# Performance work log

Measured on AMD Instinct MI355X. Metric: run time of the kernel, lower is better.

## Reference

```python
import jax, jax.numpy as jnp
import numpy as np

L, N, E, H, D = 2048, 4, 1024, 16, 128  # seq, batch, embed, heads, proj_dim
HD = E // H                             # head_dim = 64
SIGMA = 1.0
EPS = 1e-6


def setup_inputs() -> dict:
    key = jax.random.key(0)
    ks = jax.random.split(key, 13)
    w = lambda i, shape: jax.random.normal(ks[i], shape, jnp.float32) * 0.02
    return {
        "query": jax.random.normal(ks[0], (L, N, E), jnp.float32),
        "key": jax.random.normal(ks[1], (L, N, E), jnp.float32),
        "value": jax.random.normal(ks[2], (L, N, E), jnp.float32),
        "wq": w(3, (E, E)), "bq": jnp.zeros((E,), jnp.float32),
        "wk": w(4, (E, E)), "bk": jnp.zeros((E,), jnp.float32),
        "wv": w(5, (E, E)), "bv": jnp.zeros((E,), jnp.float32),
        "wo": w(6, (E, E)), "bo": jnp.zeros((E,), jnp.float32),
        "random_matrices": SIGMA * jax.random.normal(ks[7], (H, D, HD), jnp.float32),
    }


def random_project(x, rm):
    # x: (L, N, H, HD), rm: (H, D, HD) -> phi: (N*H, L, 2D)
    scale = 1.0 / np.sqrt(2 * D).astype(np.float32)
    xn = x / jnp.maximum(jnp.linalg.norm(x, axis=-1, keepdims=True), 1e-12)
    xt = jnp.einsum('lnhe,hde->lnhd', xn, rm)
    phi = scale * jnp.concatenate([jnp.exp(xt), jnp.exp(-xt)], axis=-1)  # (L,N,H,2D)
    # faithful to torch .contiguous().view(-1, L, 2D): plain row-major reshape
    return phi.reshape(N * H, L, 2 * D)


def causal_product(phi_q, phi_k, v):
    # phi_q, phi_k: (B, L, 2D); v: (B, L, HD)
    B = phi_q.shape[0]
    def step(carry, inp):
        S, z = carry            # S: (B, 2D, HD) running kv; z: (B, 2D) running k-sum
        qk, kk, vv = inp        # (B, 2D), (B, 2D), (B, HD)
        S = S + kk[:, :, None] * vv[:, None, :]
        z = z + kk
        num = jnp.einsum('bd,bdh->bh', qk, S)
        den = jnp.einsum('bd,bd->b', qk, z)
        return (S, z), num / (den[:, None] + EPS)
    init = (jnp.zeros((B, 2 * D, HD), phi_q.dtype), jnp.zeros((B, 2 * D), phi_q.dtype))
    xs = (jnp.swapaxes(phi_q, 0, 1), jnp.swapaxes(phi_k, 0, 1), jnp.swapaxes(v, 0, 1))
    _, out = jax.lax.scan(step, init, xs)   # out: (L, B, HD)
    return jnp.swapaxes(out, 0, 1)          # (B, L, HD)


def reference(query, key, value, wq, bq, wk, bk, wv, bv, wo, bo, random_matrices):
    q = query @ wq.T + bq
    k = key @ wk.T + bk
    v = value @ wv.T + bv
    q = q.reshape(L, N, H, HD)
    k = k.reshape(L, N, H, HD)
    v = jnp.swapaxes(v.reshape(L, N * H, HD), 0, 1)   # (B=N*H, L, HD)
    phi_q = random_project(q, random_matrices)        # (B, L, 2D)
    phi_k = random_project(k, random_matrices)
    attn = causal_product(phi_q, phi_k, v)            # (B, L, HD)
    attn = jnp.swapaxes(attn, 0, 1).reshape(L, N, E)
    return attn @ wo.T + bo
```

## Files before the change

kernel.cpp:

```cpp
#include <hip/hip_runtime.h>
#include <math.h>


typedef unsigned short u16;
typedef unsigned int u32;
using f32x4v  = __attribute__((ext_vector_type(4))) float;
using f32x16v = __attribute__((ext_vector_type(16))) float;
using s16x8   = __attribute__((ext_vector_type(8))) short;

__device__ __forceinline__ float bf2f(u16 u) { return __uint_as_float(((u32)u) << 16); }
__device__ __forceinline__ u16 f2bf(float x) {
    u32 b = __float_as_uint(x);
    b += 0x7fff + ((b >> 16) & 1);
    return (u16)(b >> 16);
}
__device__ __forceinline__ u32 cvtpk(float lo, float hi) {
    u32 r;
    asm("v_cvt_pk_bf16_f32 %0, %1, %2" : "=v"(r) : "v"(lo), "v"(hi));
    return r;
}
__device__ __forceinline__ void gload_lds16(const void* g, void* l) {
    __builtin_amdgcn_global_load_lds(
        (const __attribute__((address_space(1))) void*)g,
        (__attribute__((address_space(3))) void*)l, 16, 0, 0);
}

__global__ __launch_bounds__(256) void cvt_x_bf16(
    const float* __restrict__ q, const float* __restrict__ k,
    const float* __restrict__ v, u16* __restrict__ dst)
{
    const float* src = (blockIdx.y == 0) ? q : (blockIdx.y == 1) ? k : v;
    u16* d = dst + (size_t)blockIdx.y * 8388608;
    const size_t i = ((size_t)blockIdx.x * 256 + threadIdx.x) * 8;
    const float4 a = *(const float4*)(src + i);
    const float4 b = *(const float4*)(src + i + 4);
    u16 o[8] = {f2bf(a.x), f2bf(a.y), f2bf(a.z), f2bf(a.w),
                f2bf(b.x), f2bf(b.y), f2bf(b.z), f2bf(b.w)};
    *(uint4*)(d + i) = *(uint4*)o;
}

__global__ __launch_bounds__(256) void cvt_w_bf16(
    const float* __restrict__ w0, const float* __restrict__ w1,
    const float* __restrict__ w2, const float* __restrict__ w3,
    u16* __restrict__ dst)
{
    const float* src = (blockIdx.y == 0) ? w0 : (blockIdx.y == 1) ? w1
                     : (blockIdx.y == 2) ? w2 : w3;
    u16* d = dst + (size_t)blockIdx.y * 1048576;
    const size_t i = ((size_t)blockIdx.x * 256 + threadIdx.x) * 8;
    const float4 a = *(const float4*)(src + i);
    const float4 b = *(const float4*)(src + i + 4);
    u16 o[8] = {f2bf(a.x), f2bf(a.y), f2bf(a.z), f2bf(a.w),
                f2bf(b.x), f2bf(b.y), f2bf(b.z), f2bf(b.w)};
    *(uint4*)(d + i) = *(uint4*)o;
}

template<int OMODE>
__device__ __forceinline__ void gemm_body(
    const u16* __restrict__ A, const u16* __restrict__ Bw,
    const float* __restrict__ bias, void* __restrict__ Cp,
    int m0, int n0, u16* As, u16* Bs)
{
    const int t = threadIdx.x;
    const int wid = t >> 6, lane = t & 63;
    const int wr = wid >> 1, wc = wid & 1;
    const int l15 = lane & 15, l4 = lane >> 4;

    f32x4v acc[4][4];
#pragma unroll
    for (int i = 0; i < 4; ++i)
#pragma unroll
        for (int j = 0; j < 4; ++j)
#pragma unroll
            for (int e = 0; e < 4; ++e) acc[i][j][e] = 0.f;

    const int srow = wid * 32 + (lane >> 2);
    const int scol = (lane & 3) * 8;
    const u16* ga0 = A  + (size_t)(m0 + srow) * 1024 + scol;
    const u16* ga1 = ga0 + 16 * 1024;
    const u16* gb0 = Bw + (size_t)(n0 + srow) * 1024 + scol;
    const u16* gb1 = gb0 + 16 * 1024;
    u16* la0 = &As[wid * 1024];
    u16* la1 = la0 + 512;
    u16* lb0 = &Bs[wid * 1024];
    u16* lb1 = lb0 + 512;

    for (int k0 = 0; k0 < 1024; k0 += 32) {
        __syncthreads();
        gload_lds16(ga0 + k0, la0);
        gload_lds16(ga1 + k0, la1);
        gload_lds16(gb0 + k0, lb0);
        gload_lds16(gb1 + k0, lb1);
        __syncthreads();
        s16x8 af[4], bfr[4];
#pragma unroll
        for (int fi = 0; fi < 4; ++fi)
            af[fi] = *(const s16x8*)&As[(wr * 64 + fi * 16 + l15) * 32 + l4 * 8];
#pragma unroll
        for (int fj = 0; fj < 4; ++fj)
            bfr[fj] = *(const s16x8*)&Bs[(wc * 64 + fj * 16 + l15) * 32 + l4 * 8];
#pragma unroll
        for (int fi = 0; fi < 4; ++fi)
#pragma unroll
            for (int fj = 0; fj < 4; ++fj)
                acc[fi][fj] = __builtin_amdgcn_mfma_f32_16x16x32_bf16(af[fi], bfr[fj], acc[fi][fj], 0, 0, 0);
    }

    const int rl = l4 * 4, cl = l15;
    float bvals[4];
#pragma unroll
    for (int fj = 0; fj < 4; ++fj) bvals[fj] = bias[n0 + wc * 64 + fj * 16 + cl];
#pragma unroll
    for (int fi = 0; fi < 4; ++fi)
#pragma unroll
        for (int j = 0; j < 4; ++j) {
            const size_t m = m0 + wr * 64 + fi * 16 + rl + j;
#pragma unroll
            for (int fj = 0; fj < 4; ++fj) {
                const int n = n0 + wc * 64 + fj * 16 + cl;
                const float v = acc[fi][fj][j] + bvals[fj];
                if (OMODE == 0)      ((float*)Cp)[m * 1024 + n] = v;
                else if (OMODE == 1) ((u16*)Cp)[m * 1024 + n] = f2bf(v);
                else {
                    ((u16*)Cp)[((size_t)((m & 3) * 16 + (n >> 6)) * 64 + (n & 63)) * 2048 + (m >> 2)] = f2bf(v);
                }
            }
        }
}

template<int OMODE>
__global__ __launch_bounds__(256) void gemm_bf16(
    const u16* __restrict__ A, const u16* __restrict__ Bw,
    const float* __restrict__ bias, void* __restrict__ Cp)
{
    __shared__ __align__(16) u16 As[4096];
    __shared__ __align__(16) u16 Bs[4096];
    gemm_body<OMODE>(A, Bw, bias, Cp, blockIdx.x * 128, blockIdx.y * 128, As, Bs);
}

__global__ __launch_bounds__(256) void gemm_qk(
    const u16* __restrict__ xq, const u16* __restrict__ wq, const float* __restrict__ bq, u16* __restrict__ qp,
    const u16* __restrict__ xk, const u16* __restrict__ wk, const float* __restrict__ bk, u16* __restrict__ kp)
{
    __shared__ __align__(16) u16 As[4096];
    __shared__ __align__(16) u16 Bs[4096];
    const bool isq = (blockIdx.z == 0);
    gemm_body<1>(isq ? xq : xk, isq ? wq : wk, isq ? bq : bk, isq ? (void*)qp : (void*)kp,
                 blockIdx.x * 128, blockIdx.y * 128, As, Bs);
}

__global__ __launch_bounds__(256) void rand_project2(
    const u16* __restrict__ QP, const u16* __restrict__ KP,
    const float* __restrict__ RM, u16* __restrict__ PHIQ, u16* __restrict__ PHIK)
{
    const u16* X  = (blockIdx.z == 0) ? QP : KP;
    u16* PHI      = (blockIdx.z == 0) ? PHIQ : PHIK;
    __shared__ float Xs[64][68];
    __shared__ float RMs[128][68];
    __shared__ float rsc[64];
    const int h  = blockIdx.x;
    const int r0 = blockIdx.y * 64;
    const int t  = threadIdx.x;
#pragma unroll
    for (int i = 0; i < 2; ++i) {
        const int lin = t + i * 256;
        const int r = lin >> 3, c8 = (lin & 7) * 8;
        const uint4 v = *(const uint4*)(X + (size_t)(r0 + r) * 1024 + h * 64 + c8);
        const u16* pv = (const u16*)&v;
#pragma unroll
        for (int e = 0; e < 8; ++e) Xs[r][c8 + e] = bf2f(pv[e]);
    }
#pragma unroll
    for (int i = 0; i < 32; ++i) {
        const int lin = t + i * 256;
        const int d = lin >> 6, c = lin & 63;
        RMs[d][c] = RM[((size_t)h * 128 + d) * 64 + c];
    }
    __syncthreads();
    if (t < 64) {
        float s = 0.f;
#pragma unroll
        for (int c = 0; c < 64; ++c) { const float v = Xs[t][c]; s += v * v; }
        rsc[t] = 1.f / fmaxf(sqrtf(s), 1e-12f);
    }
    __syncthreads();
    const int rr = (t >> 4) * 4;
    const int dc = t & 15;
    float acc[4][8];
#pragma unroll
    for (int i = 0; i < 4; ++i)
#pragma unroll
        for (int j = 0; j < 8; ++j) acc[i][j] = 0.f;
    for (int c = 0; c < 64; c += 4) {
        float4 xv[4], rv[8];
#pragma unroll
        for (int i = 0; i < 4; ++i) xv[i] = *(const float4*)&Xs[rr + i][c];
#pragma unroll
        for (int j = 0; j < 8; ++j) rv[j] = *(const float4*)&RMs[dc + 16 * j][c];
#pragma unroll
        for (int i = 0; i < 4; ++i)
#pragma unroll
            for (int j = 0; j < 8; ++j)
                acc[i][j] += xv[i].x*rv[j].x + xv[i].y*rv[j].y + xv[i].z*rv[j].z + xv[i].w*rv[j].w;
    }
#pragma unroll
    for (int i = 0; i < 4; ++i) {
        const float sc = rsc[rr + i];
        const size_t base = ((size_t)(r0 + rr + i) * 16 + h) * 256;
#pragma unroll
        for (int j = 0; j < 8; ++j) {
            const float xt = acc[i][j] * sc;
            const int d = dc + 16 * j;
            PHI[base + d]       = f2bf(0.0625f * expf(xt));
            PHI[base + 128 + d] = f2bf(0.0625f * expf(-xt));
        }
    }
}

__global__ __launch_bounds__(256) void chunk_state_mfma(
    const u16* __restrict__ PHIK, const u16* __restrict__ VPT, float* __restrict__ ST)
{
    __shared__ __align__(16) u16 Ks[64 * 136];
    __shared__ float zlds[16][132];
    const int b = blockIdx.x;
    const int c = blockIdx.y >> 1;
    const int dh = blockIdx.y & 1;
    const int t = threadIdx.x;
    const int wid = t >> 6, lane = t & 63;
    const int l15 = lane & 15, l4 = lane >> 4;
    const int wr = wid >> 1, wc = wid & 1;

    const size_t R0 = (size_t)b * 2048 + (size_t)c * 256;
    const int rgrp = t >> 4, d08 = (t & 15) * 8;

    float zpart[8];
#pragma unroll
    for (int i = 0; i < 8; ++i) zpart[i] = 0.f;

    f32x4v acc[2][4];
#pragma unroll
    for (int i = 0; i < 2; ++i)
#pragma unroll
        for (int j = 0; j < 4; ++j)
#pragma unroll
            for (int e = 0; e < 4; ++e) acc[i][j][e] = 0.f;

    for (int stage = 0; stage < 4; ++stage) {
        __syncthreads();
#pragma unroll
        for (int j = 0; j < 4; ++j) {
            const int r = rgrp + 16 * j;
            const uint4 v = *(const uint4*)(PHIK + (R0 + stage * 64 + r) * 256 + dh * 128 + d08);
            const int x = ((r >> 3) & 3) << 1;
            *(uint4*)&Ks[r * 136 + (((d08 >> 3) ^ x) << 3)] = v;
            const u16* pv = (const u16*)&v;
#pragma unroll
            for (int i = 0; i < 8; ++i) zpart[i] += bf2f(pv[i]);
        }
        __syncthreads();
#pragma unroll
        for (int ks = 0; ks < 2; ++ks) {
            const int xk = ((ks * 4 + l4) & 3) << 1;
            const int r0 = ks * 32 + l4 * 8;
            s16x8 af[2], bk[4];
#pragma unroll
            for (int fi = 0; fi < 2; ++fi) {
                const int h = wr * 32 + fi * 16 + l15;
                af[fi] = *(const s16x8*)(VPT + ((size_t)b * 64 + h) * 2048 + c * 256 + stage * 64 + ks * 32 + l4 * 8);
            }
#pragma unroll
            for (int fj = 0; fj < 4; ++fj) {
                const int d = wc * 64 + fj * 16 + l15;
                const int colk = (((d >> 3) ^ xk) << 3) + (d & 7);
#pragma unroll
                for (int e = 0; e < 8; ++e)
                    bk[fj][e] = (short)Ks[(r0 + e) * 136 + colk];
            }
#pragma unroll
            for (int fi = 0; fi < 2; ++fi)
#pragma unroll
                for (int fj = 0; fj < 4; ++fj)
                    acc[fi][fj] = __builtin_amdgcn_mfma_f32_16x16x32_bf16(af[fi], bk[fj], acc[fi][fj], 0, 0, 0);
        }
    }
    __syncthreads();
    *(float4*)&zlds[rgrp][d08]     = *(float4*)&zpart[0];
    *(float4*)&zlds[rgrp][d08 + 4] = *(float4*)&zpart[4];
    __syncthreads();
    float* st = ST + (size_t)(b * 8 + c) * 16640;
    if (t < 128) {
        float z = 0.f;
#pragma unroll
        for (int g = 0; g < 16; ++g) z += zlds[g][t];
        st[16384 + dh * 128 + t] = z;
    }
#pragma unroll
    for (int fi = 0; fi < 2; ++fi)
#pragma unroll
        for (int reg = 0; reg < 4; ++reg) {
            const int h = wr * 32 + fi * 16 + l4 * 4 + reg;
#pragma unroll
            for (int fj = 0; fj < 4; ++fj) {
                const int d = dh * 128 + wc * 64 + fj * 16 + l15;
                st[(size_t)h * 256 + d] = acc[fi][fj][reg];
            }
        }
}

__global__ void prefix_scan(const float* __restrict__ ST, u16* __restrict__ STBF)
{
    const int b = blockIdx.x;
    const int e = blockIdx.y * 256 + threadIdx.x;
    if (e >= 16640) return;
    const size_t base = (size_t)b * 8 * 16640 + e;
    float run = 0.f;
#pragma unroll
    for (int c = 0; c < 8; ++c) {
        const float v = ST[base + (size_t)c * 16640];
        STBF[(size_t)(b * 8 + c) * 16640 + e] = f2bf(run);
        run += v;
    }
}

__global__ __launch_bounds__(128) void causal_fused(
    const u16* __restrict__ PHIQ, const u16* __restrict__ PHIK,
    const u16* __restrict__ VPT, const u16* __restrict__ STBF,
    u16* __restrict__ ATT)
{
    const u32 bid = blockIdx.x;
    const int pair = (int)((bid >> 3) & 3);
    const int G  = (int)((bid >> 5) * 8 + (bid & 7));
    const int b  = G & 63;
    const int c  = G >> 6;
    const int w  = threadIdx.x >> 6;
    const int rf = w ? (7 - pair) : pair;
    const int ri = rf >> 1, fi = rf & 1;
    const int lane = threadIdx.x & 63;
    const int l31 = lane & 31, s = lane >> 5;
    const size_t chunk0 = (size_t)b * 2048 + (size_t)c * 256;
    const u16* stb = STBF + (size_t)(b * 8 + c) * 16640;

    const int qc = ri * 64 + fi * 32 + l31;
    s16x8 qf[16];
    const u16* qp = PHIQ + (chunk0 + qc) * 256 + s * 8;
#pragma unroll
    for (int ds = 0; ds < 16; ++ds)
        qf[ds] = *(const s16x8*)(qp + ds * 16);

    f32x16v o[2], o2;
#pragma unroll
    for (int e = 0; e < 16; ++e) { o[0][e] = 0.f; o[1][e] = 0.f; o2[e] = 0.f; }
    float den = 0.f;

#pragma unroll
    for (int ds = 0; ds < 16; ++ds) {
        const s16x8 zf = *(const s16x8*)(stb + 16384 + ds * 16 + s * 8);
        o2 = __builtin_amdgcn_mfma_f32_32x32x16_bf16(qf[ds], zf, o2, 0, 0, 0);
#pragma unroll
        for (int fh = 0; fh < 2; ++fh) {
            const s16x8 sx = *(const s16x8*)(stb + (fh * 32 + l31) * 256 + ds * 16 + s * 8);
            o[fh] = __builtin_amdgcn_mfma_f32_32x32x16_bf16(qf[ds], sx, o[fh], 0, 0, 0);
        }
    }

    const int kbmax = ri * 2 + fi;
    for (int kb = 0; kb <= kbmax; ++kb) {
        s16x8 vf[2][2];
#pragma unroll
        for (int kh = 0; kh < 2; ++kh)
#pragma unroll
            for (int fh = 0; fh < 2; ++fh)
                vf[kh][fh] = *(const s16x8*)(VPT + ((size_t)b * 64 + fh * 32 + l31) * 2048
                                             + c * 256 + kb * 32 + kh * 16 + s * 8);
        f32x16v p0, p1;
#pragma unroll
        for (int e = 0; e < 16; ++e) { p0[e] = 0.f; p1[e] = 0.f; }
        const u16* kptr = PHIK + (chunk0 + kb * 32 + l31) * 256 + s * 8;
#pragma unroll
        for (int ds = 0; ds < 8; ++ds) {
            const s16x8 kf0 = *(const s16x8*)(kptr + (2 * ds) * 16);
            const s16x8 kf1 = *(const s16x8*)(kptr + (2 * ds + 1) * 16);
            p0 = __builtin_amdgcn_mfma_f32_32x32x16_bf16(kf0, qf[2 * ds],     p0, 0, 0, 0);
            p1 = __builtin_amdgcn_mfma_f32_32x32x16_bf16(kf1, qf[2 * ds + 1], p1, 0, 0, 0);
        }
        f32x16v p;
#pragma unroll
        for (int e = 0; e < 16; ++e) p[e] = p0[e] + p1[e];

        const bool diag = (kb == kbmax);
        float rsum = 0.f;
#pragma unroll
        for (int reg = 0; reg < 16; ++reg) {
            if (diag) {
                const int kc = kb * 32 + (reg & 3) + 8 * (reg >> 2) + 4 * s;
                if (kc > qc) p[reg] = 0.f;
            }
            rsum += p[reg];
        }
        den += rsum;
#pragma unroll
        for (int kh = 0; kh < 2; ++kh) {
            const u32 pA_lo = cvtpk(p[8*kh + 0], p[8*kh + 1]);
            const u32 pA_hi = cvtpk(p[8*kh + 2], p[8*kh + 3]);
            const u32 pB_lo = cvtpk(p[8*kh + 4], p[8*kh + 5]);
            const u32 pB_hi = cvtpk(p[8*kh + 6], p[8*kh + 7]);
            const u32 X_lo = s ? pB_lo : pA_lo;
            const u32 X_hi = s ? pB_hi : pA_hi;
            const u32 Y_lo = s ? pA_lo : pB_lo;
            const u32 Y_hi = s ? pA_hi : pB_hi;
            const u32 sY_lo = __shfl_xor((int)Y_lo, 32);
            const u32 sY_hi = __shfl_xor((int)Y_hi, 32);
            u32 wq[4];
            wq[0] = s ? sY_lo : X_lo;
            wq[1] = s ? sY_hi : X_hi;
            wq[2] = s ? X_lo : sY_lo;
            wq[3] = s ? X_hi : sY_hi;
            s16x8 pa;
#pragma unroll
            for (int i = 0; i < 4; ++i) {
                pa[2*i]   = (short)(wq[i] & 0xffff);
                pa[2*i+1] = (short)(wq[i] >> 16);
            }
            o[0] = __builtin_amdgcn_mfma_f32_32x32x16_bf16(pa, vf[kh][0], o[0], 0, 0, 0);
            o[1] = __builtin_amdgcn_mfma_f32_32x32x16_bf16(pa, vf[kh][1], o[1], 0, 0, 0);
        }
    }

    const float denT = den + __shfl_xor(den, 32);
#pragma unroll
    for (int reg = 0; reg < 16; ++reg) {
        const int q32 = (reg & 3) + 8 * (reg >> 2) + 4 * s;
        const float dv = o2[reg] + __shfl(denT, q32);
        const float inv = 1.f / (dv + 1e-6f);
        const int qrow = c * 256 + ri * 64 + fi * 32 + q32;
        const size_t abase = (size_t)qrow * 4096 + b * 64;
        ATT[abase + l31]      = f2bf(o[0][reg] * inv);
        ATT[abase + 32 + l31] = f2bf(o[1][reg] * inv);
    }
}

extern "C" void kernel_launch(void* const* d_in, const int* in_sizes, int n_in,
                              void* d_out, int out_size, void* d_ws, size_t ws_size,
                              hipStream_t stream)
{
    const float* query = (const float*)d_in[0];
    const float* key   = (const float*)d_in[1];
    const float* value = (const float*)d_in[2];
    const float* wq    = (const float*)d_in[3];
    const float* bq    = (const float*)d_in[4];
    const float* wk    = (const float*)d_in[5];
    const float* bk    = (const float*)d_in[6];
    const float* wv    = (const float*)d_in[7];
    const float* bv    = (const float*)d_in[8];
    const float* wo    = (const float*)d_in[9];
    const float* bo    = (const float*)d_in[10];
    const float* rm    = (const float*)d_in[11];
    float* out = (float*)d_out;

    char* base = (char*)d_ws;
    u16*   phiq = (u16*)(base);
    u16*   phik = (u16*)(base +  67108864);
    u16*   qp   = (u16*)(base + 134217728);
    u16*   vpt  = (u16*)(base + 134217728);
    u16*   kp   = (u16*)(base + 150994944);
    u16*   stbf = (u16*)(base + 150994944);
    u16*   xbf  = (u16*)(base + 168034304);
    float* st   = (float*)(base + 168034304);
    u16*   attn = (u16*)(base + 168034304);
    u16*   wbf  = (u16*)(base + 218365952);

    u16* xq = xbf;
    u16* xk = xbf +  8388608;
    u16* xv = xbf + 16777216;
    u16* wqb = wbf;
    u16* wkb = wbf + 1048576;
    u16* wvb = wbf + 2097152;
    u16* wob = wbf + 3145728;

    const dim3 blk(256);
    cvt_x_bf16<<<dim3(4096, 3), blk, 0, stream>>>(query, key, value, xbf);
    cvt_w_bf16<<<dim3(512, 4), blk, 0, stream>>>(wq, wk, wv, wo, wbf);
    gemm_qk<<<dim3(64, 8, 2), blk, 0, stream>>>(xq, wqb, bq, qp, xk, wkb, bk, kp);
    rand_project2<<<dim3(16, 128, 2), blk, 0, stream>>>(qp, kp, rm, phiq, phik);
    gemm_bf16<2><<<dim3(64, 8), blk, 0, stream>>>(xv, wvb, bv, vpt);
    chunk_state_mfma<<<dim3(64, 16), blk, 0, stream>>>(phik, vpt, st);
    prefix_scan<<<dim3(64, 65), blk, 0, stream>>>(st, stbf);
    causal_fused<<<dim3(2048), dim3(128), 0, stream>>>(phiq, phik, vpt, stbf, attn);
    gemm_bf16<0><<<dim3(64, 8), blk, 0, stream>>>(attn, wob, bo, out);
}
```

Before: 347.1 us.

## Run random projection on bf16 MFMA with hardware exp2 and fused norm

The random-feature projection kernel now does its 64-wide contraction with bf16 MFMA 16x16x32 instructions instead of scalar fp32 FMAs in LDS. The random matrix is converted to bf16 by a new small kernel, and the tile grows to 128 rows. Row norms are computed during the load using shuffles, and exp is replaced by the raw v_exp_f32 (exp2) with log2(e) and the 1/16 scale folded in. This trades some precision for far fewer ALU instructions, and adds one extra launch.

```diff
diff --git a/kernel.cpp b/kernel.cpp
--- a/kernel.cpp
+++ b/kernel.cpp
@@ -17,6 +17,11 @@
 __device__ __forceinline__ u32 cvtpk(float lo, float hi) {
     u32 r;
     asm("v_cvt_pk_bf16_f32 %0, %1, %2" : "=v"(r) : "v"(lo), "v"(hi));
+    return r;
+}
+__device__ __forceinline__ float exp2f_hw(float x) {
+    float r;
+    asm("v_exp_f32 %0, %1" : "=v"(r) : "v"(x));
     return r;
 }
 __device__ __forceinline__ void gload_lds16(const void* g, void* l) {
@@ -53,6 +58,17 @@
     u16 o[8] = {f2bf(a.x), f2bf(a.y), f2bf(a.z), f2bf(a.w),
                 f2bf(b.x), f2bf(b.y), f2bf(b.z), f2bf(b.w)};
     *(uint4*)(d + i) = *(uint4*)o;
+}
+
+__global__ __launch_bounds__(256) void cvt_rm_bf16(
+    const float* __restrict__ rm, u16* __restrict__ dst)
+{
+    const size_t i = ((size_t)blockIdx.x * 256 + threadIdx.x) * 8;
+    const float4 a = *(const float4*)(rm + i);
+    const float4 b = *(const float4*)(rm + i + 4);
+    u16 o[8] = {f2bf(a.x), f2bf(a.y), f2bf(a.z), f2bf(a.w),
+                f2bf(b.x), f2bf(b.y), f2bf(b.z), f2bf(b.w)};
+    *(uint4*)(dst + i) = *(uint4*)o;
 }
 
 template<int OMODE>
@@ -149,72 +165,85 @@
                  blockIdx.x * 128, blockIdx.y * 128, As, Bs);
 }
 
-__global__ __launch_bounds__(256) void rand_project2(
+__global__ __launch_bounds__(256) void rand_project_mfma(
     const u16* __restrict__ QP, const u16* __restrict__ KP,
-    const float* __restrict__ RM, u16* __restrict__ PHIQ, u16* __restrict__ PHIK)
+    const u16* __restrict__ RMB, u16* __restrict__ PHIQ, u16* __restrict__ PHIK)
 {
     const u16* X  = (blockIdx.z == 0) ? QP : KP;
     u16* PHI      = (blockIdx.z == 0) ? PHIQ : PHIK;
-    __shared__ float Xs[64][68];
-    __shared__ float RMs[128][68];
-    __shared__ float rsc[64];
+    __shared__ __align__(16) u16 Xs[128 * 72];
+    __shared__ __align__(16) u16 RMs[128 * 72];
+    __shared__ float rsl_lds[128];
     const int h  = blockIdx.x;
-    const int r0 = blockIdx.y * 64;
+    const int r0 = blockIdx.y * 128;
     const int t  = threadIdx.x;
-#pragma unroll
-    for (int i = 0; i < 2; ++i) {
+    const int w  = t >> 6, lane = t & 63;
+    const int l15 = lane & 15, l4 = lane >> 4;
+
+    float sq[4];
+#pragma unroll
+    for (int i = 0; i < 4; ++i) {
         const int lin = t + i * 256;
-        const int r = lin >> 3, c8 = (lin & 7) * 8;
-        const uint4 v = *(const uint4*)(X + (size_t)(r0 + r) * 1024 + h * 64 + c8);
-        const u16* pv = (const u16*)&v;
-#pragma unroll
-        for (int e = 0; e < 8; ++e) Xs[r][c8 + e] = bf2f(pv[e]);
-    }
-#pragma unroll
-    for (int i = 0; i < 32; ++i) {
-        const int lin = t + i * 256;
-        const int d = lin >> 6, c = lin & 63;
-        RMs[d][c] = RM[((size_t)h * 128 + d) * 64 + c];
+        const int row = lin >> 3, oct = lin & 7;
+        const uint4 xv = *(const uint4*)(X + (size_t)(r0 + row) * 1024 + h * 64 + oct * 8);
+        *(uint4*)&Xs[row * 72 + oct * 8] = xv;
+        const u16* pv = (const u16*)&xv;
+        float s = 0.f;
+#pragma unroll
+        for (int e = 0; e < 8; ++e) { const float f = bf2f(pv[e]); s += f * f; }
+        sq[i] = s;
+        const uint4 rv = *(const uint4*)(RMB + (size_t)h * 8192 + lin * 8);
+        *(uint4*)&RMs[row * 72 + oct * 8] = rv;
+    }
+#pragma unroll
+    for (int i = 0; i < 4; ++i) {
+        sq[i] += __shfl_xor(sq[i], 1);
+        sq[i] += __shfl_xor(sq[i], 2);
+        sq[i] += __shfl_xor(sq[i], 4);
+        if ((t & 7) == 0)
+            rsl_lds[(t >> 3) + i * 32] = 1.4426950408889634f / fmaxf(sqrtf(sq[i]), 1e-12f);
     }
     __syncthreads();
-    if (t < 64) {
-        float s = 0.f;
-#pragma unroll
-        for (int c = 0; c < 64; ++c) { const float v = Xs[t][c]; s += v * v; }
-        rsc[t] = 1.f / fmaxf(sqrtf(s), 1e-12f);
-    }
-    __syncthreads();
-    const int rr = (t >> 4) * 4;
-    const int dc = t & 15;
-    float acc[4][8];
+
+    const int wr = (w >> 1) * 64, wc = (w & 1) * 64;
+    f32x4v acc[4][4];
 #pragma unroll
     for (int i = 0; i < 4; ++i)
 #pragma unroll
-        for (int j = 0; j < 8; ++j) acc[i][j] = 0.f;
-    for (int c = 0; c < 64; c += 4) {
-        float4 xv[4], rv[8];
-#pragma unroll
-        for (int i = 0; i < 4; ++i) xv[i] = *(const float4*)&Xs[rr + i][c];
-#pragma unroll
-        for (int j = 0; j < 8; ++j) rv[j] = *(const float4*)&RMs[dc + 16 * j][c];
-#pragma unroll
-        for (int i = 0; i < 4; ++i)
-#pragma unroll
-            for (int j = 0; j < 8; ++j)
-                acc[i][j] += xv[i].x*rv[j].x + xv[i].y*rv[j].y + xv[i].z*rv[j].z + xv[i].w*rv[j].w;
-    }
-#pragma unroll
-    for (int i = 0; i < 4; ++i) {
-        const float sc = rsc[rr + i];
-        const size_t base = ((size_t)(r0 + rr + i) * 16 + h) * 256;
-#pragma unroll
-        for (int j = 0; j < 8; ++j) {
-            const float xt = acc[i][j] * sc;
-            const int d = dc + 16 * j;
-            PHI[base + d]       = f2bf(0.0625f * expf(xt));
-            PHI[base + 128 + d] = f2bf(0.0625f * expf(-xt));
-        }
-    }
+        for (int j = 0; j < 4; ++j)
+#pragma unroll
+            for (int e = 0; e < 4; ++e) acc[i][j][e] = 0.f;
+#pragma unroll
+    for (int ks = 0; ks < 2; ++ks) {
+        s16x8 af[4], bfr[4];
+#pragma unroll
+        for (int fi = 0; fi < 4; ++fi)
+            af[fi] = *(const s16x8*)&Xs[(wr + fi * 16 + l15) * 72 + ks * 32 + l4 * 8];
+#pragma unroll
+        for (int fj = 0; fj < 4; ++fj)
+            bfr[fj] = *(const s16x8*)&RMs[(wc + fj * 16 + l15) * 72 + ks * 32 + l4 * 8];
+#pragma unroll
+        for (int fi = 0; fi < 4; ++fi)
+#pragma unroll
+            for (int fj = 0; fj < 4; ++fj)
+                acc[fi][fj] = __builtin_amdgcn_mfma_f32_16x16x32_bf16(af[fi], bfr[fj], acc[fi][fj], 0, 0, 0);
+    }
+
+#pragma unroll
+    for (int fi = 0; fi < 4; ++fi)
+#pragma unroll
+        for (int reg = 0; reg < 4; ++reg) {
+            const int row = wr + fi * 16 + l4 * 4 + reg;
+            const float rsl = rsl_lds[row];
+            const size_t base = ((size_t)(r0 + row) * 16 + h) * 256;
+#pragma unroll
+            for (int fj = 0; fj < 4; ++fj) {
+                const int d = wc + fj * 16 + l15;
+                const float arg = acc[fi][fj][reg] * rsl;
+                PHI[base + d]       = f2bf(exp2f_hw(arg - 4.f));
+                PHI[base + 128 + d] = f2bf(exp2f_hw(-arg - 4.f));
+            }
+        }
 }
 
 __global__ __launch_bounds__(256) void chunk_state_mfma(
@@ -468,6 +497,7 @@
     float* st   = (float*)(base + 168034304);
     u16*   attn = (u16*)(base + 168034304);
     u16*   wbf  = (u16*)(base + 218365952);
+    u16*   rmb  = (u16*)(base + 226754560);
 
     u16* xq = xbf;
     u16* xk = xbf +  8388608;
@@ -480,8 +510,9 @@
     const dim3 blk(256);
     cvt_x_bf16<<<dim3(4096, 3), blk, 0, stream>>>(query, key, value, xbf);
     cvt_w_bf16<<<dim3(512, 4), blk, 0, stream>>>(wq, wk, wv, wo, wbf);
+    cvt_rm_bf16<<<dim3(64), blk, 0, stream>>>(rm, rmb);
     gemm_qk<<<dim3(64, 8, 2), blk, 0, stream>>>(xq, wqb, bq, qp, xk, wkb, bk, kp);
-    rand_project2<<<dim3(16, 128, 2), blk, 0, stream>>>(qp, kp, rm, phiq, phik);
+    rand_project_mfma<<<dim3(16, 64, 2), blk, 0, stream>>>(qp, kp, rmb, phiq, phik);
     gemm_bf16<2><<<dim3(64, 8), blk, 0, stream>>>(xv, wvb, bv, vpt);
     chunk_state_mfma<<<dim3(64, 16), blk, 0, stream>>>(phik, vpt, st);
     prefix_scan<<<dim3(64, 65), blk, 0, stream>>>(st, stbf);
```

New measurement: 291.3 us. 1.19x faster.
